# Kernel optimization log

Hardware: AMD Instinct MI355X
Metric: run time of the kernel (lower is better)

Reference implementation:

```python
import jax, jax.numpy as jnp
import numpy as np

# NOTE: create_positions() is not defined in the source repo snippet. We implement the
# standard duration-model convention: per-frame offset within its phoneme segment,
# i.e. positions[b,t] = t - start_frame(segment containing t). mode is unused here.

B, N, T, D = 8, 512, 8192, 256


def setup_inputs() -> dict:
    key = jax.random.key(0)
    rng = np.random.default_rng(0)
    dur = rng.integers(8, 24, size=(B, N)).astype(np.int64)
    # force every row to sum exactly to T so max(sum(durations)) == T (static shape)
    dur[:, -1] += T - dur.sum(axis=1)
    assert (dur > 0).all()
    durations = jnp.asarray(dur, dtype=jnp.int32)
    x = jax.random.normal(key, (B, N, D), dtype=jnp.float32)
    return {"x": x, "durations": durations}


def reference(x, durations):
    durf = durations.astype(jnp.float32)                      # [B,N]
    e = jnp.cumsum(durf, axis=-1)                             # segment end frames [B,N]
    c = e - 0.5 * durf                                        # segment centers   [B,N]
    # T is static by construction (rows of durations all sum to the same total)
    t = jnp.arange(T, dtype=jnp.float32)                      # [T]
    # weights[b,n,t] = 1 iff |t - c + 1e-6| < dur/2 (zeros-then-fill in torch == this)
    w = jnp.abs(t[None, None, :] - c[:, :, None] + 1e-6)      # [B,N,T]
    weights = (w < durf[:, :, None] * 0.5).astype(jnp.float32)
    # out[b,t,d] = sum_n weights[b,n,t] * x[b,n,d]  (== weights.transpose(1,2) @ x)
    out = jnp.einsum('bnt,bnd->btd', weights, x)              # [B,T,D]
    # create_positions: offset of each frame within its phoneme segment
    starts = e - durf                                         # [B,N]
    positions = t[None, :] - jnp.einsum('bnt,bn->bt', weights, starts)  # [B,T]
    return positions, out, weights
```

## Files before the change

### kernel.cpp

```cpp
#include <hip/hip_runtime.h>
#include <math.h>

#define BB 8
#define NN 512
#define TT 8192
#define DD 256

#define THREADS 256
#define BLOCKS  2048
#define FRAMES  32
#define MAXROWS 6

typedef float v4f __attribute__((ext_vector_type(4)));

__global__ void __launch_bounds__(THREADS)
fused_kernel(const float* __restrict__ x,
             const int* __restrict__ dur,
             float* __restrict__ positions,
             float* __restrict__ outp,
             float* __restrict__ w) {
    __shared__ int s_end[NN + 1];
    __shared__ unsigned char s_cov[NN];
    __shared__ short seg_blk[FRAMES];
    __shared__ int s_nlo, s_nhi;
    __shared__ float xs[(MAXROWS + 1) * DD];

    const int bid  = blockIdx.x;
    const int b    = bid >> 8;
    const int sub  = bid & 255;
    const int tid  = threadIdx.x;
    const int lane = tid & 63;

    if (tid < 64) {
        const int4 da = *(const int4*)(dur + b * NN + 8 * lane);
        const int4 db = *(const int4*)(dur + b * NN + 8 * lane + 4);
        int d[8] = {da.x, da.y, da.z, da.w, db.x, db.y, db.z, db.w};
        int pre[8], s = 0;
        #pragma unroll
        for (int j = 0; j < 8; ++j) { pre[j] = s; s += d[j]; }
        int incl = s;
        #pragma unroll
        for (int off = 1; off < 64; off <<= 1) {
            const int v = __shfl_up(incl, off, 64);
            if (lane >= off) incl += v;
        }
        const int base = incl - s;
        #pragma unroll
        for (int j = 0; j < 8; ++j) {
            const int n = 8 * lane + j;
            s_end[n] = base + pre[j];
            const float h = 0.5f * (float)d[j];
            s_cov[n] = (fabsf(1e-6f - h) < h) ? 1 : 0;
        }
        if (lane == 63) s_end[NN] = incl;
    }
    __syncthreads();

    const int f0 = sub * FRAMES;
    if (tid < FRAMES) {
        const int t = f0 + tid;
        int lo = 0, hi = NN - 1;
        while (lo < hi) {
            const int mid = (lo + hi) >> 1;
            if (t < s_end[mid + 1]) hi = mid; else lo = mid + 1;
        }
        const int st   = s_end[lo];
        const bool unc = (t == st) && !s_cov[lo];
        seg_blk[tid] = (short)(unc ? -1 : lo);
        positions[b * TT + t] = unc ? (float)t : (float)(t - st);
        if (tid == 0)          s_nlo = lo;
        if (tid == FRAMES - 1) s_nhi = lo;
    }
    __syncthreads();

    const int nlo   = s_nlo;
    const int nrows = s_nhi - nlo + 1;
    for (int idx = tid; idx < (nrows + 1) * (DD / 4); idx += THREADS) {
        const int r  = idx >> 6;
        const int d4 = (idx & 63) << 2;
        v4f v = (v4f)(0.0f);
        if (r < nrows)
            v = *(const v4f*)(x + (((size_t)b * NN + nlo + r) * DD + d4));
        *(v4f*)(xs + r * DD + d4) = v;
    }
    __syncthreads();

    float* oc = outp + ((size_t)b * TT + f0) * DD;
    #pragma unroll
    for (int k = 0; k < FRAMES * (DD / 4) / THREADS; ++k) {
        const int idx = k * THREADS + tid;
        const int f   = idx >> 6;
        const int d4  = (idx & 63) << 2;
        const int sg  = seg_blk[f];
        const int row = (sg < 0) ? nrows : (sg - nlo);
        const v4f v = *(const v4f*)(xs + row * DD + d4);
        *(v4f*)(oc + ((size_t)idx << 2)) = v;
    }

    const int n0 = sub * 2;
    #pragma unroll
    for (int r = 0; r < 2; ++r) {
        const int n  = n0 + r;
        const int rs = s_end[n] + (s_cov[n] ? 0 : 1);
        const int re = s_end[n + 1];
        const int a  = rs & ~31;
        const int e  = (re + 31) & ~31;
        float* wrow = w + (((size_t)b * NN + n) << 13);
        for (int t = a + (tid << 2); t < e; t += THREADS * 4) {
            v4f o;
            o.x = (t     >= rs && t     < re) ? 1.0f : 0.0f;
            o.y = (t + 1 >= rs && t + 1 < re) ? 1.0f : 0.0f;
            o.z = (t + 2 >= rs && t + 2 < re) ? 1.0f : 0.0f;
            o.w = (t + 3 >= rs && t + 3 < re) ? 1.0f : 0.0f;
            *(v4f*)(wrow + t) = o;
        }
    }
}

extern "C" void kernel_launch(void* const* d_in, const int* in_sizes, int n_in,
                              void* d_out, int out_size, void* d_ws, size_t ws_size,
                              hipStream_t stream) {
    const float* x  = (const float*)d_in[0];
    const int* dur  = (const int*)d_in[1];

    float* pos  = (float*)d_out;
    float* outp = pos + (size_t)BB * TT;
    float* w    = outp + (size_t)BB * TT * DD;

    hipMemsetAsync(w, 0, (size_t)BB * NN * TT * sizeof(float), stream);
    fused_kernel<<<BLOCKS, THREADS, 0, stream>>>(x, dur, pos, outp, w);
}
```

Baseline: 36.49 us.

## Write full weight rows in-kernel and drop the separate memset

The kernel now writes every element of its two weight rows, zeros included, inside the same loop that writes the output frames. That makes the host-side memset of the whole weight tensor unnecessary, so it is removed. This saves a separate launch and merges the memset's write stream with the kernel's stores. In exchange, every block now issues 8 KB-row stores per row through its own threads instead of relying on the driver's fill path.

```diff
diff --git a/kernel.cpp b/kernel.cpp
--- a/kernel.cpp
+++ b/kernel.cpp
@@ -14,11 +14,11 @@
 typedef float v4f __attribute__((ext_vector_type(4)));
 
 __global__ void __launch_bounds__(THREADS)
-fused_kernel(const float* __restrict__ x,
-             const int* __restrict__ dur,
-             float* __restrict__ positions,
-             float* __restrict__ outp,
-             float* __restrict__ w) {
+merged_kernel(const float* __restrict__ x,
+              const int* __restrict__ dur,
+              float* __restrict__ positions,
+              float* __restrict__ outp,
+              float* __restrict__ w) {
     __shared__ int s_end[NN + 1];
     __shared__ unsigned char s_cov[NN];
     __shared__ short seg_blk[FRAMES];
@@ -85,9 +85,17 @@
     }
     __syncthreads();
 
+    const int n0  = sub * 2;
+    const int rs0 = s_end[n0]     + (s_cov[n0]     ? 0 : 1);
+    const int re0 = s_end[n0 + 1];
+    const int rs1 = s_end[n0 + 1] + (s_cov[n0 + 1] ? 0 : 1);
+    const int re1 = s_end[n0 + 2];
     float* oc = outp + ((size_t)b * TT + f0) * DD;
+    float* w0 = w + (((size_t)b * NN + n0) << 13);
+    float* w1 = w0 + TT;
+
     #pragma unroll
-    for (int k = 0; k < FRAMES * (DD / 4) / THREADS; ++k) {
+    for (int k = 0; k < 8; ++k) {
         const int idx = k * THREADS + tid;
         const int f   = idx >> 6;
         const int d4  = (idx & 63) << 2;
@@ -95,25 +103,18 @@
         const int row = (sg < 0) ? nrows : (sg - nlo);
         const v4f v = *(const v4f*)(xs + row * DD + d4);
         *(v4f*)(oc + ((size_t)idx << 2)) = v;
-    }
-
-    const int n0 = sub * 2;
-    #pragma unroll
-    for (int r = 0; r < 2; ++r) {
-        const int n  = n0 + r;
-        const int rs = s_end[n] + (s_cov[n] ? 0 : 1);
-        const int re = s_end[n + 1];
-        const int a  = rs & ~31;
-        const int e  = (re + 31) & ~31;
-        float* wrow = w + (((size_t)b * NN + n) << 13);
-        for (int t = a + (tid << 2); t < e; t += THREADS * 4) {
-            v4f o;
-            o.x = (t     >= rs && t     < re) ? 1.0f : 0.0f;
-            o.y = (t + 1 >= rs && t + 1 < re) ? 1.0f : 0.0f;
-            o.z = (t + 2 >= rs && t + 2 < re) ? 1.0f : 0.0f;
-            o.w = (t + 3 >= rs && t + 3 < re) ? 1.0f : 0.0f;
-            *(v4f*)(wrow + t) = o;
-        }
+        const int t = idx << 2;
+        v4f o0, o1;
+        o0.x = (t     >= rs0 && t     < re0) ? 1.0f : 0.0f;
+        o0.y = (t + 1 >= rs0 && t + 1 < re0) ? 1.0f : 0.0f;
+        o0.z = (t + 2 >= rs0 && t + 2 < re0) ? 1.0f : 0.0f;
+        o0.w = (t + 3 >= rs0 && t + 3 < re0) ? 1.0f : 0.0f;
+        *(v4f*)(w0 + t) = o0;
+        o1.x = (t     >= rs1 && t     < re1) ? 1.0f : 0.0f;
+        o1.y = (t + 1 >= rs1 && t + 1 < re1) ? 1.0f : 0.0f;
+        o1.z = (t + 2 >= rs1 && t + 2 < re1) ? 1.0f : 0.0f;
+        o1.w = (t + 3 >= rs1 && t + 3 < re1) ? 1.0f : 0.0f;
+        *(v4f*)(w1 + t) = o1;
     }
 }
 
@@ -127,6 +128,5 @@
     float* outp = pos + (size_t)BB * TT;
     float* w    = outp + (size_t)BB * TT * DD;
 
-    hipMemsetAsync(w, 0, (size_t)BB * NN * TT * sizeof(float), stream);
-    fused_kernel<<<BLOCKS, THREADS, 0, stream>>>(x, dur, pos, outp, w);
+    merged_kernel<<<BLOCKS, THREADS, 0, stream>>>(x, dur, pos, outp, w);
 }
```

Result: faster. 33.90 us (-7.1%).
